# Kernel optimization log

Measured on AMD Instinct MI355X. Metric: run time of the kernel, lower is better.

Reference implementation:

```python
import jax, jax.numpy as jnp
import numpy as np

# yolov5 non_max_suppression defaults (from forward's input_parameters.get defaults)
CONF_THRES = 0.25
IOU_THRES = 0.45
MAX_DET = 1000        # max detections returned per image
TOP_K = 4096          # fixed candidate count entering greedy NMS (jit-friendly stand-in for max_nms)
MAX_WH = 7680.0       # per-class box offset so NMS is class-aware (yolov5 trick)


def setup_inputs() -> dict:
    key = jax.random.key(0)
    k1, k2, k3, k4 = jax.random.split(key, 4)
    B, N, NC = 16, 25200, 80  # 640x640 yolov5 -> 25200 anchors, 80 COCO classes
    xy = jax.random.uniform(k1, (B, N, 2)) * 640.0            # box centers in pixels
    wh = jax.random.uniform(k2, (B, N, 2)) * 160.0 + 4.0       # box sizes
    obj = jax.random.uniform(k3, (B, N, 1))                    # objectness
    cls = jax.random.uniform(k4, (B, N, NC))                   # class scores
    pred = jnp.concatenate([xy, wh, obj, cls], axis=-1)        # [B, N, 85]
    return {"pred": pred}


def _xywh2xyxy(x):
    xy, wh = x[..., :2], x[..., 2:4]
    return jnp.concatenate([xy - wh * 0.5, xy + wh * 0.5], axis=-1)


def _iou_one_vs_all(box, boxes):
    # box [4], boxes [K,4], xyxy
    lt = jnp.maximum(box[:2], boxes[:, :2])
    rb = jnp.minimum(box[2:], boxes[:, 2:])
    wh = jnp.clip(rb - lt, 0.0)
    inter = wh[:, 0] * wh[:, 1]
    a1 = (box[2] - box[0]) * (box[3] - box[1])
    a2 = (boxes[:, 2] - boxes[:, 0]) * (boxes[:, 3] - boxes[:, 1])
    return inter / (a1 + a2 - inter + 1e-7)


def _nms_single(pred):
    # pred [N, 5+nc] raw yolov5 output for one image
    obj = pred[:, 4:5]
    scores_all = pred[:, 5:] * obj                 # conf = obj_conf * cls_conf
    conf = scores_all.max(axis=-1)                 # best-class confidence [N]
    cls = scores_all.argmax(axis=-1).astype(pred.dtype)
    boxes = _xywh2xyxy(pred[:, :4])                # [N,4] xyxy

    valid = conf > CONF_THRES
    s = jnp.where(valid, conf, -1.0)
    order = jnp.argsort(-s)[:TOP_K]                # top candidates by score
    b = boxes[order]                               # [K,4]
    sc = s[order]                                  # [K]
    c = cls[order]                                 # [K]
    ob = b + c[:, None] * MAX_WH                   # class-offset boxes for class-aware NMS

    ar = jnp.arange(TOP_K)

    def step(supp, i):
        alive = (~supp[i]) & (sc[i] > 0.0)
        iou = _iou_one_vs_all(ob[i], ob)
        supp = supp | (alive & (iou > IOU_THRES) & (ar > i))
        return supp, alive

    _, keep = jax.lax.scan(step, jnp.zeros(TOP_K, dtype=bool), ar)

    fs = jnp.where(keep, sc, -1.0)
    idx = jnp.argsort(-fs)[:MAX_DET]               # kept boxes, score-sorted
    det = jnp.concatenate([b[idx], fs[idx][:, None], c[idx][:, None]], axis=-1)  # [max_det,6]
    ok = fs[idx] > 0.0
    return jnp.where(ok[:, None], det, 0.0)        # zero-padded [max_det, 6] (x1,y1,x2,y2,conf,cls)


def reference(pred):
    # [B, max_det, 6] padded detections per image
    return jax.vmap(_nms_single)(pred)
```

## Files before the change

### kernel.cpp

```cpp
#include <hip/hip_runtime.h>

#define BATCH  16
#define NPRED  25200
#define NCLS   80
#define CDIM   85
#define TOPK   4096
#define NPAD   28672
#define NCHUNK 7
#define MAXDET 1000
#define CONF_T 0.25f
#define IOU_T  0.45f
#define MAXWH  7680.0f

typedef unsigned long long u64;
typedef unsigned int u32;
typedef unsigned short u16;
typedef unsigned char u8;

__device__ __forceinline__ u64 umax64(u64 a, u64 b) { return a > b ? a : b; }
__device__ __forceinline__ u64 umin64(u64 a, u64 b) { return a < b ? a : b; }

__device__ __forceinline__ void cx_u64(u64* a, int i, int p, bool desc) {
    u64 x = a[i], y = a[p];
    if (desc ? (x < y) : (x > y)) { a[i] = y; a[p] = x; }
}


__device__ void hybrid_sort4096_desc(u64 r[4], u64* a) {
    const int tid = threadIdx.x;
    for (int k = 2; k <= 4096; k <<= 1) {
        if (k >= 512) {
            int jmax = (k >> 1) > 2048 ? 2048 : (k >> 1);
#pragma unroll
            for (int e = 0; e < 4; ++e) a[4 * tid + e] = r[e];
            __syncthreads();
            for (int j = jmax; j >= 256; j >>= 1) {
#pragma unroll
                for (int t2 = 0; t2 < 2; ++t2) {
                    int q = (t2 << 10) | tid;
                    int i = ((q & ~(j - 1)) << 1) | (q & (j - 1));
                    cx_u64(a, i, i | j, (i & k) == 0);
                }
                __syncthreads();
            }
#pragma unroll
            for (int e = 0; e < 4; ++e) r[e] = a[4 * tid + e];
            __syncthreads();
        }
        {
            int jstart = (k >> 1) > 128 ? 128 : (k >> 1);
            bool desc = (((4 * tid) & k) == 0);
            for (int j = jstart; j >= 4; j >>= 1) {
                int m = j >> 2;
                bool take_max = (((tid & m) == 0) == desc);
#pragma unroll
                for (int e = 0; e < 4; ++e) {
                    u64 v = __shfl_xor(r[e], m, 64);
                    r[e] = take_max ? umax64(r[e], v) : umin64(r[e], v);
                }
            }
        }
        if (k >= 4) {
            bool desc = (((4 * tid) & k) == 0);
            u64 x0 = r[0], x2 = r[2];
            r[0] = desc ? umax64(x0, x2) : umin64(x0, x2);
            r[2] = desc ? umin64(x0, x2) : umax64(x0, x2);
            u64 x1 = r[1], x3 = r[3];
            r[1] = desc ? umax64(x1, x3) : umin64(x1, x3);
            r[3] = desc ? umin64(x1, x3) : umax64(x1, x3);
        }
        {
            bool d01 = (((4 * tid + 0) & k) == 0);
            bool d23 = (((4 * tid + 2) & k) == 0);
            u64 x0 = r[0], x1 = r[1];
            r[0] = d01 ? umax64(x0, x1) : umin64(x0, x1);
            r[1] = d01 ? umin64(x0, x1) : umax64(x0, x1);
            u64 x2 = r[2], x3 = r[3];
            r[2] = d23 ? umax64(x2, x3) : umin64(x2, x3);
            r[3] = d23 ? umin64(x2, x3) : umax64(x2, x3);
        }
    }
}

__device__ void hybrid_merge4096_desc(u64 r[4], u64* a) {
    const int tid = threadIdx.x;
#pragma unroll
    for (int e = 0; e < 4; ++e) a[4 * tid + e] = r[e];
    __syncthreads();
    for (int j = 2048; j >= 256; j >>= 1) {
#pragma unroll
        for (int t2 = 0; t2 < 2; ++t2) {
            int q = (t2 << 10) | tid;
            int i = ((q & ~(j - 1)) << 1) | (q & (j - 1));
            cx_u64(a, i, i | j, true);
        }
        __syncthreads();
    }
#pragma unroll
    for (int e = 0; e < 4; ++e) r[e] = a[4 * tid + e];
    for (int j = 128; j >= 4; j >>= 1) {
        int m = j >> 2;
        bool take_max = ((tid & m) == 0);
#pragma unroll
        for (int e = 0; e < 4; ++e) {
            u64 v = __shfl_xor(r[e], m, 64);
            r[e] = take_max ? umax64(r[e], v) : umin64(r[e], v);
        }
    }
    {
        u64 x0 = r[0], x2 = r[2];
        r[0] = umax64(x0, x2); r[2] = umin64(x0, x2);
        u64 x1 = r[1], x3 = r[3];
        r[1] = umax64(x1, x3); r[3] = umin64(x1, x3);
    }
    {
        u64 x0 = r[0], x1 = r[1];
        r[0] = umax64(x0, x1); r[1] = umin64(x0, x1);
        u64 x2 = r[2], x3 = r[3];
        r[2] = umax64(x2, x3); r[3] = umin64(x2, x3);
    }
}


__global__ __launch_bounds__(256) void k1_score(const float* __restrict__ pred,
                                                u64* __restrict__ keys) {
    const int lane = threadIdx.x & 63;
    const int l16 = lane & 15;
    const long long gw = (long long)blockIdx.x * 4 + (threadIdx.x >> 6);
    const long long rowIdx = gw * 4 + (lane >> 4);
    const int b = (int)(rowIdx / NPAD);
    const int n = (int)(rowIdx - (long long)b * NPAD);
    u64 key = 0ull;
    if (n < NPRED) {
        const float* row = pred + ((long long)b * NPRED + n) * CDIM;
        float obj = row[4];
        u64 m = 0ull;
#pragma unroll
        for (int k = 0; k < 5; ++k) {
            int c = l16 + 16 * k;
            float v = row[5 + c] * obj;
            u64 mk = ((u64)(__float_as_uint(v) | 0x80000000u) << 32) | (u64)(u32)(NCLS - 1 - c);
            if (mk > m) m = mk;
        }
#pragma unroll
        for (int o = 8; o > 0; o >>= 1) {
            u64 other = __shfl_xor(m, o, 64);
            if (other > m) m = other;
        }
        float best = __uint_as_float((u32)(m >> 32) & 0x7FFFFFFFu);
        int cls = (NCLS - 1) - (int)(m & 0x7Fu);
        float s = (best > CONF_T) ? best : -1.0f;
        u32 u = __float_as_uint(s);
        u32 ord = (u & 0x80000000u) ? ~u : (u | 0x80000000u);
        key = ((u64)ord << 32) | ((u64)(u32)(NPAD - 1 - n) << 7) | (u64)(u32)cls;
    }
    if (l16 == 0) keys[(long long)b * NPAD + n] = key;
}


__global__ __launch_bounds__(1024) void k2a_sortchunk(u64* __restrict__ keys) {
    __shared__ u64 a[4096];
    const int tid = threadIdx.x;
    u64* kb = keys + (long long)blockIdx.x * 4096;
    u64 r[4];
#pragma unroll
    for (int e = 0; e < 4; ++e) r[e] = kb[4 * tid + e];
    hybrid_sort4096_desc(r, a);
#pragma unroll
    for (int e = 0; e < 4; ++e) kb[4 * tid + e] = r[e];
}


__global__ __launch_bounds__(1024) void k2m_merge(u64* __restrict__ keys, int stride) {
    __shared__ u64 a[4096];
    const int tid = threadIdx.x;
    const int b = blockIdx.x;
    const int c0 = blockIdx.y * 2 * stride;
    const u64* A = keys + (long long)b * NPAD + (long long)c0 * 4096;
    const u64* B = keys + (long long)b * NPAD + (long long)(c0 + stride) * 4096;
    u64 r[4];
#pragma unroll
    for (int e = 0; e < 4; ++e) {
        int i = 4 * tid + e;
        r[e] = umax64(A[i], B[4095 - i]);
    }
    hybrid_merge4096_desc(r, a);
    u64* O = keys + (long long)b * NPAD + (long long)c0 * 4096;
#pragma unroll
    for (int e = 0; e < 4; ++e) O[4 * tid + e] = r[e];
}


__global__ __launch_bounds__(256) void k3a_build(const float* __restrict__ pred,
                                                 const u64* __restrict__ keys,
                                                 float4* __restrict__ ob,
                                                 u8* __restrict__ clsb,
                                                 u32* __restrict__ count) {
    const int idx = blockIdx.x * 256 + threadIdx.x;
    const int b = idx >> 12;
    const int r = idx & 4095;
    u64 key = keys[(long long)b * NPAD + r];
    u32 hi = (u32)(key >> 32);
    u8 c = 0xFF;
    if (hi > 0x80000000u) {
        int n = (NPAD - 1) - (int)((key >> 7) & 0x7FFFu);
        int ci = (int)(key & 0x7Fu);
        const float* row = pred + ((long long)b * NPRED + n) * CDIM;
        float x = row[0], y = row[1], w = row[2], h = row[3];
        float off = (float)ci * MAXWH;
        float4 o;
        o.x = (x - w * 0.5f) + off;
        o.y = (y - h * 0.5f) + off;
        o.z = (x + w * 0.5f) + off;
        o.w = (y + h * 0.5f) + off;
        ob[idx] = o;
        c = (u8)ci;
        atomicAdd(&count[b * NCLS + ci], 1u);
    }
    clsb[idx] = c;
}


__global__ __launch_bounds__(64) void k3g_gather(const u8* __restrict__ clsb,
                                                 const u32* __restrict__ count,
                                                 u32* __restrict__ startg,
                                                 u16* __restrict__ segIdx) {
    const int b = blockIdx.x;
    const int c = blockIdx.y;
    const int lane = threadIdx.x;
    u32 s = (lane < c) ? count[b * NCLS + lane] : 0u;
    if (lane + 64 < c) s += count[b * NCLS + 64 + lane];
#pragma unroll
    for (int o = 32; o > 0; o >>= 1) s += __shfl_xor(s, o, 64);
    if (lane == 0) startg[b * NCLS + c] = s;
    const u32 base = (u32)b * 4096u;
    u32 pos = s;
    const u64 lt = (1ull << lane) - 1ull;
    for (int it = 0; it < 64; ++it) {
        u8 cc = clsb[base + it * 64 + lane];
        u64 m = __ballot(cc == (u8)c);
        if (cc == (u8)c) {
            int ofs = __popcll(m & lt);
            segIdx[base + pos + ofs] = (u16)(it * 64 + lane);
        }
        pos += (u32)__popcll(m);
    }
}


__global__ __launch_bounds__(64) void k3n_nms(const float4* __restrict__ ob,
                                              const u16* __restrict__ segIdx,
                                              const u32* __restrict__ count,
                                              const u32* __restrict__ startg,
                                              u8* __restrict__ keep,
                                              u8* gsupp_) {
    const int b = blockIdx.x;
    const int c = blockIdx.y;
    const int lane = threadIdx.x;
    const int n = (int)count[b * NCLS + c];
    if (n == 0) return;
    const u32 base = startg[b * NCLS + c];
    __shared__ float4 sbox[1024];
    __shared__ u16 sidx[1024];
    __shared__ u8 ssupp_[1024];
    volatile u8* ssupp = ssupp_;
    volatile u8* gsupp = gsupp_ + b * 4096 + base;
    const float4* obb = ob + b * 4096;
    const u16* seg = segIdx + b * 4096 + base;

    for (int j = lane; j < n && j < 1024; j += 64) {
        int r = seg[j];
        sidx[j] = (u16)r;
        sbox[j] = obb[r];
        ssupp_[j] = 0;
    }
    __syncthreads();

    {
#pragma clang fp contract(off)
        for (int ii = 0; ii < n; ++ii) {
            bool sup = (ii < 1024) ? (ssupp[ii] != 0) : (gsupp[ii] != 0);
            if (sup) continue;
            int ri = (ii < 1024) ? (int)sidx[ii] : (int)seg[ii];
            if (lane == 0) keep[b * 4096 + ri] = 1;
            float4 bi = (ii < 1024) ? sbox[ii] : obb[seg[ii]];
            float a1 = (bi.z - bi.x) * (bi.w - bi.y);
            for (int jj = ii + 1 + lane; jj < n; jj += 64) {
                float4 bj = (jj < 1024) ? sbox[jj] : obb[seg[jj]];
                float ltx = fmaxf(bi.x, bj.x);
                float lty = fmaxf(bi.y, bj.y);
                float rbx = fminf(bi.z, bj.z);
                float rby = fminf(bi.w, bj.w);
                float ww = fmaxf(rbx - ltx, 0.0f);
                float hh = fmaxf(rby - lty, 0.0f);
                float inter = ww * hh;
                float a2 = (bj.z - bj.x) * (bj.w - bj.y);
                float iou = inter / (((a1 + a2) - inter) + 1e-7f);
                if (iou > IOU_T) {
                    if (jj < 1024) ssupp[jj] = 1; else gsupp[jj] = 1;
                }
            }
            __syncthreads();
        }
    }
}


__global__ __launch_bounds__(256) void k3o_out(const float* __restrict__ pred,
                                               const u64* __restrict__ keys,
                                               const u8* __restrict__ keep,
                                               float* __restrict__ out) {
    const int b = blockIdx.x;
    const int tid = threadIdx.x;
    __shared__ u64 words[64];
    __shared__ int wpre[64];
    float* outb = out + (long long)b * MAXDET * 6;
    for (int i = tid; i < MAXDET * 6; i += 256) outb[i] = 0.0f;
    const u8* kp = keep + b * 4096;
    if (tid < 64) {
        u64 w = 0ull;
        const u64* k8 = (const u64*)(kp + tid * 64);
#pragma unroll
        for (int q = 0; q < 8; ++q) {
            u64 v = k8[q];
#pragma unroll
            for (int bb = 0; bb < 8; ++bb)
                if ((v >> (8 * bb)) & 0xFFull) w |= 1ull << (q * 8 + bb);
        }
        words[tid] = w;
    }
    __syncthreads();
    if (tid == 0) {
        int run = 0;
        for (int t = 0; t < 64; ++t) { wpre[t] = run; run += __popcll(words[t]); }
    }
    __syncthreads();
    const u64* kb = keys + (long long)b * NPAD;
    for (int r = tid; r < 4096; r += 256) {
        int wd = r >> 6;
        if ((words[wd] >> (r & 63)) & 1ull) {
            int pos = wpre[wd] + __popcll(words[wd] & ((1ull << (r & 63)) - 1ull));
            if (pos < MAXDET) {
                u64 key = kb[r];
                u32 hi = (u32)(key >> 32);
                int n = (NPAD - 1) - (int)((key >> 7) & 0x7FFFu);
                const float* row = pred + ((long long)b * NPRED + n) * CDIM;
                float x = row[0], y = row[1], w2 = row[2], h = row[3];
                float* o = outb + pos * 6;
                o[0] = x - w2 * 0.5f;
                o[1] = y - h * 0.5f;
                o[2] = x + w2 * 0.5f;
                o[3] = y + h * 0.5f;
                o[4] = __uint_as_float(hi & 0x7FFFFFFFu);
                o[5] = (float)(key & 0x7Fu);
            }
        }
    }
}


extern "C" void kernel_launch(void* const* d_in, const int* in_sizes, int n_in,
                              void* d_out, int out_size, void* d_ws, size_t ws_size,
                              hipStream_t stream) {
    const float* pred = (const float*)d_in[0];
    float* out = (float*)d_out;

    char* ws = (char*)d_ws;
    u64* keys   = (u64*)ws;
    float4* ob  = (float4*)(ws + 3670016);
    u8* clsb    = (u8*)(ws + 4718592);
    u16* segIdx = (u16*)(ws + 4784128);
    u32* startg = (u32*)(ws + 4915200);
    u32* count  = (u32*)(ws + 4920320);
    u8* keep    = (u8*)(ws + 4925440);
    u8* gsupp   = (u8*)(ws + 4990976);
    (void)hipMemsetAsync(ws + 4920320, 0, 136192, stream);

    hipLaunchKernelGGL(k1_score, dim3(BATCH * NPAD / 16), dim3(256), 0, stream, pred, keys);
    hipLaunchKernelGGL(k2a_sortchunk, dim3(BATCH * NCHUNK), dim3(1024), 0, stream, keys);
    hipLaunchKernelGGL(k2m_merge, dim3(BATCH, 3), dim3(1024), 0, stream, keys, 1);
    hipLaunchKernelGGL(k2m_merge, dim3(BATCH, 2), dim3(1024), 0, stream, keys, 2);
    hipLaunchKernelGGL(k2m_merge, dim3(BATCH, 1), dim3(1024), 0, stream, keys, 4);
    hipLaunchKernelGGL(k3a_build, dim3(BATCH * TOPK / 256), dim3(256), 0, stream,
                       pred, keys, ob, clsb, count);
    hipLaunchKernelGGL(k3g_gather, dim3(BATCH, NCLS), dim3(64), 0, stream,
                       clsb, count, startg, segIdx);
    hipLaunchKernelGGL(k3n_nms, dim3(BATCH, NCLS), dim3(64), 0, stream,
                       ob, segIdx, count, startg, keep, gsupp);
    hipLaunchKernelGGL(k3o_out, dim3(BATCH), dim3(256), 0, stream, pred, keys, keep, out);
}
```

Baseline: 304.6 us.

## Replace full candidate sort with histogram threshold selection plus single 4096 sort

The score kernel now builds a per-image 4096-bucket histogram of valid scores with global atomics. A new per-image kernel scans that histogram to find the bucket holding the 4096th candidate, compacts the keys above that bucket into shared memory, and sorts the boundary bucket separately to fill the remainder. Only the selected 4096 keys are then bitonic-sorted, replacing the multi-chunk sort and merge passes over all 28672 padded keys. The trade-offs are atomic contention on the histogram and a single block per image doing the compaction, plus a boundary bucket capped at 1024 entries.

```diff
diff --git a/kernel.cpp b/kernel.cpp
--- a/kernel.cpp
+++ b/kernel.cpp
@@ -5,12 +5,12 @@
 #define NCLS   80
 #define CDIM   85
 #define TOPK   4096
-#define NPAD   28672
-#define NCHUNK 7
+#define NBUCK  4096
 #define MAXDET 1000
 #define CONF_T 0.25f
 #define IOU_T  0.45f
 #define MAXWH  7680.0f
+#define ORD_BASE 0xBE800000u
 
 typedef unsigned long long u64;
 typedef unsigned int u32;
@@ -82,128 +82,196 @@
     }
 }
 
-__device__ void hybrid_merge4096_desc(u64 r[4], u64* a) {
-    const int tid = threadIdx.x;
-#pragma unroll
-    for (int e = 0; e < 4; ++e) a[4 * tid + e] = r[e];
-    __syncthreads();
-    for (int j = 2048; j >= 256; j >>= 1) {
-#pragma unroll
-        for (int t2 = 0; t2 < 2; ++t2) {
-            int q = (t2 << 10) | tid;
-            int i = ((q & ~(j - 1)) << 1) | (q & (j - 1));
-            cx_u64(a, i, i | j, true);
-        }
-        __syncthreads();
-    }
-#pragma unroll
-    for (int e = 0; e < 4; ++e) r[e] = a[4 * tid + e];
-    for (int j = 128; j >= 4; j >>= 1) {
-        int m = j >> 2;
-        bool take_max = ((tid & m) == 0);
-#pragma unroll
-        for (int e = 0; e < 4; ++e) {
-            u64 v = __shfl_xor(r[e], m, 64);
-            r[e] = take_max ? umax64(r[e], v) : umin64(r[e], v);
-        }
-    }
-    {
-        u64 x0 = r[0], x2 = r[2];
-        r[0] = umax64(x0, x2); r[2] = umin64(x0, x2);
-        u64 x1 = r[1], x3 = r[3];
-        r[1] = umax64(x1, x3); r[3] = umin64(x1, x3);
-    }
-    {
-        u64 x0 = r[0], x1 = r[1];
-        r[0] = umax64(x0, x1); r[1] = umin64(x0, x1);
-        u64 x2 = r[2], x3 = r[3];
-        r[2] = umax64(x2, x3); r[3] = umin64(x2, x3);
+__device__ void wave_sort256_desc(u64 r[4]) {
+    const int lane = threadIdx.x & 63;
+    for (int k = 2; k <= 256; k <<= 1) {
+        int jstart = (k >> 1) > 128 ? 128 : (k >> 1);
+        bool desc = (((4 * lane) & k) == 0);
+        for (int j = jstart; j >= 4; j >>= 1) {
+            int m = j >> 2;
+            bool take_max = (((lane & m) == 0) == desc);
+#pragma unroll
+            for (int e = 0; e < 4; ++e) {
+                u64 v = __shfl_xor(r[e], m, 64);
+                r[e] = take_max ? umax64(r[e], v) : umin64(r[e], v);
+            }
+        }
+        if (k >= 4) {
+            u64 x0 = r[0], x2 = r[2];
+            r[0] = desc ? umax64(x0, x2) : umin64(x0, x2);
+            r[2] = desc ? umin64(x0, x2) : umax64(x0, x2);
+            u64 x1 = r[1], x3 = r[3];
+            r[1] = desc ? umax64(x1, x3) : umin64(x1, x3);
+            r[3] = desc ? umin64(x1, x3) : umax64(x1, x3);
+        }
+        {
+            bool d01 = (((4 * lane + 0) & k) == 0);
+            bool d23 = (((4 * lane + 2) & k) == 0);
+            u64 x0 = r[0], x1 = r[1];
+            r[0] = d01 ? umax64(x0, x1) : umin64(x0, x1);
+            r[1] = d01 ? umin64(x0, x1) : umax64(x0, x1);
+            u64 x2 = r[2], x3 = r[3];
+            r[2] = d23 ? umax64(x2, x3) : umin64(x2, x3);
+            r[3] = d23 ? umin64(x2, x3) : umax64(x2, x3);
+        }
     }
 }
 
 
 __global__ __launch_bounds__(256) void k1_score(const float* __restrict__ pred,
-                                                u64* __restrict__ keys) {
+                                                u64* __restrict__ keys,
+                                                u32* __restrict__ ghist) {
     const int lane = threadIdx.x & 63;
     const int l16 = lane & 15;
     const long long gw = (long long)blockIdx.x * 4 + (threadIdx.x >> 6);
     const long long rowIdx = gw * 4 + (lane >> 4);
-    const int b = (int)(rowIdx / NPAD);
-    const int n = (int)(rowIdx - (long long)b * NPAD);
-    u64 key = 0ull;
-    if (n < NPRED) {
-        const float* row = pred + ((long long)b * NPRED + n) * CDIM;
-        float obj = row[4];
-        u64 m = 0ull;
-#pragma unroll
-        for (int k = 0; k < 5; ++k) {
-            int c = l16 + 16 * k;
-            float v = row[5 + c] * obj;
-            u64 mk = ((u64)(__float_as_uint(v) | 0x80000000u) << 32) | (u64)(u32)(NCLS - 1 - c);
-            if (mk > m) m = mk;
-        }
-#pragma unroll
-        for (int o = 8; o > 0; o >>= 1) {
-            u64 other = __shfl_xor(m, o, 64);
-            if (other > m) m = other;
-        }
+    const int b = (int)(rowIdx / NPRED);
+    const int n = (int)(rowIdx - (long long)b * NPRED);
+    const float* row = pred + rowIdx * CDIM;
+    float obj = row[4];
+    u64 m = 0ull;
+#pragma unroll
+    for (int k = 0; k < 5; ++k) {
+        int c = l16 + 16 * k;
+        float v = row[5 + c] * obj;
+        u64 mk = ((u64)(__float_as_uint(v) | 0x80000000u) << 32) | (u64)(u32)(NCLS - 1 - c);
+        if (mk > m) m = mk;
+    }
+#pragma unroll
+    for (int o = 8; o > 0; o >>= 1) {
+        u64 other = __shfl_xor(m, o, 64);
+        if (other > m) m = other;
+    }
+    if (l16 == 0) {
         float best = __uint_as_float((u32)(m >> 32) & 0x7FFFFFFFu);
         int cls = (NCLS - 1) - (int)(m & 0x7Fu);
         float s = (best > CONF_T) ? best : -1.0f;
         u32 u = __float_as_uint(s);
         u32 ord = (u & 0x80000000u) ? ~u : (u | 0x80000000u);
-        key = ((u64)ord << 32) | ((u64)(u32)(NPAD - 1 - n) << 7) | (u64)(u32)cls;
-    }
-    if (l16 == 0) keys[(long long)b * NPAD + n] = key;
-}
-
-
-__global__ __launch_bounds__(1024) void k2a_sortchunk(u64* __restrict__ keys) {
-    __shared__ u64 a[4096];
+        keys[rowIdx] = ((u64)ord << 32) | ((u64)(u32)(32767 - n) << 7) | (u64)(u32)cls;
+        if (ord > ORD_BASE)
+            atomicAdd(&ghist[b * NBUCK + ((ord - ORD_BASE - 1u) >> 12)], 1u);
+    }
+}
+
+
+__global__ __launch_bounds__(1024) void k2cs(const u64* __restrict__ keys,
+                                             const u32* __restrict__ ghist,
+                                             u64* __restrict__ topSorted) {
+    __shared__ u64 smem[4096];
+    __shared__ u64 side[1024];
+    __shared__ u32 wsum[16];
+    __shared__ int sh_T, sh_C1, sh_R, c1pos, sidepos;
+    const int b = blockIdx.x;
     const int tid = threadIdx.x;
-    u64* kb = keys + (long long)blockIdx.x * 4096;
+    const int lane = tid & 63;
+    const int wid = tid >> 6;
+
+    u32 h[4];
+    u32 tsum = 0;
+#pragma unroll
+    for (int e = 0; e < 4; ++e) {
+        h[e] = ghist[b * NBUCK + (NBUCK - 1 - (4 * tid + e))];
+        tsum += h[e];
+    }
+    u32 inc = tsum;
+    for (int o = 1; o < 64; o <<= 1) {
+        u32 v = __shfl_up(inc, o, 64);
+        if (lane >= o) inc += v;
+    }
+    if (lane == 63) wsum[wid] = inc;
+    __syncthreads();
+    if (tid == 0) {
+        u32 run = 0;
+        for (int i = 0; i < 16; ++i) { u32 t = wsum[i]; wsum[i] = run; run += t; }
+        sh_T = -1; sh_C1 = (int)run; sh_R = 0;
+        c1pos = 0; sidepos = 0;
+    }
+    __syncthreads();
+    {
+        u32 cum = wsum[wid] + (inc - tsum);
+#pragma unroll
+        for (int e = 0; e < 4; ++e) {
+            if (h[e] > 0 && cum < (u32)TOPK && cum + h[e] >= (u32)TOPK) {
+                sh_T = NBUCK - 1 - (4 * tid + e);
+                sh_C1 = (int)cum;
+                sh_R = TOPK - (int)cum;
+            }
+            cum += h[e];
+        }
+    }
+    __syncthreads();
+    const int T = sh_T, C1 = sh_C1, R = sh_R;
+
+    for (int i = tid; i < 4096; i += 1024) smem[i] = 0ull;
+    side[tid] = 0ull;
+    __syncthreads();
+    const u64* kb = keys + (long long)b * NPRED;
+    for (int n = tid; n < NPRED; n += 1024) {
+        u64 key = kb[n];
+        u32 hi = (u32)(key >> 32);
+        if (hi > ORD_BASE) {
+            int bt = (int)((hi - ORD_BASE - 1u) >> 12);
+            if (bt > T) {
+                int slot = atomicAdd(&c1pos, 1);
+                smem[slot] = key;
+            } else if (bt == T) {
+                int s2 = atomicAdd(&sidepos, 1);
+                if (s2 < 1024) side[s2] = key;
+            }
+        }
+    }
+    __syncthreads();
+
+    if (R > 0) {
+        int cntT = sidepos;
+        if (cntT <= 256) {
+            if (wid == 0) {
+                u64 r[4];
+#pragma unroll
+                for (int e = 0; e < 4; ++e) r[e] = side[4 * lane + e];
+                wave_sort256_desc(r);
+#pragma unroll
+                for (int e = 0; e < 4; ++e) side[4 * lane + e] = r[e];
+            }
+        } else {
+            for (int k = 2; k <= 1024; k <<= 1) {
+                for (int j = k >> 1; j >= 1; j >>= 1) {
+                    if (tid < 512) {
+                        int q = tid;
+                        int i = ((q & ~(j - 1)) << 1) | (q & (j - 1));
+                        cx_u64(side, i, i | j, (i & k) == 0);
+                    }
+                    __syncthreads();
+                }
+            }
+        }
+        __syncthreads();
+        if (tid < R) smem[C1 + tid] = side[tid];
+    }
+    __syncthreads();
+
     u64 r[4];
 #pragma unroll
-    for (int e = 0; e < 4; ++e) r[e] = kb[4 * tid + e];
-    hybrid_sort4096_desc(r, a);
-#pragma unroll
-    for (int e = 0; e < 4; ++e) kb[4 * tid + e] = r[e];
-}
-
-
-__global__ __launch_bounds__(1024) void k2m_merge(u64* __restrict__ keys, int stride) {
-    __shared__ u64 a[4096];
-    const int tid = threadIdx.x;
-    const int b = blockIdx.x;
-    const int c0 = blockIdx.y * 2 * stride;
-    const u64* A = keys + (long long)b * NPAD + (long long)c0 * 4096;
-    const u64* B = keys + (long long)b * NPAD + (long long)(c0 + stride) * 4096;
-    u64 r[4];
-#pragma unroll
-    for (int e = 0; e < 4; ++e) {
-        int i = 4 * tid + e;
-        r[e] = umax64(A[i], B[4095 - i]);
-    }
-    hybrid_merge4096_desc(r, a);
-    u64* O = keys + (long long)b * NPAD + (long long)c0 * 4096;
-#pragma unroll
-    for (int e = 0; e < 4; ++e) O[4 * tid + e] = r[e];
+    for (int e = 0; e < 4; ++e) r[e] = smem[4 * tid + e];
+    hybrid_sort4096_desc(r, smem);
+#pragma unroll
+    for (int e = 0; e < 4; ++e) topSorted[(long long)b * TOPK + 4 * tid + e] = r[e];
 }
 
 
 __global__ __launch_bounds__(256) void k3a_build(const float* __restrict__ pred,
-                                                 const u64* __restrict__ keys,
+                                                 const u64* __restrict__ topSorted,
                                                  float4* __restrict__ ob,
                                                  u8* __restrict__ clsb,
                                                  u32* __restrict__ count) {
     const int idx = blockIdx.x * 256 + threadIdx.x;
     const int b = idx >> 12;
-    const int r = idx & 4095;
-    u64 key = keys[(long long)b * NPAD + r];
+    u64 key = topSorted[idx];
     u32 hi = (u32)(key >> 32);
     u8 c = 0xFF;
     if (hi > 0x80000000u) {
-        int n = (NPAD - 1) - (int)((key >> 7) & 0x7FFFu);
+        int n = 32767 - (int)((key >> 7) & 0x7FFFu);
         int ci = (int)(key & 0x7Fu);
         const float* row = pred + ((long long)b * NPRED + n) * CDIM;
         float x = row[0], y = row[1], w = row[2], h = row[3];
@@ -307,7 +375,7 @@
 
 
 __global__ __launch_bounds__(256) void k3o_out(const float* __restrict__ pred,
-                                               const u64* __restrict__ keys,
+                                               const u64* __restrict__ topSorted,
                                                const u8* __restrict__ keep,
                                                float* __restrict__ out) {
     const int b = blockIdx.x;
@@ -335,7 +403,7 @@
         for (int t = 0; t < 64; ++t) { wpre[t] = run; run += __popcll(words[t]); }
     }
     __syncthreads();
-    const u64* kb = keys + (long long)b * NPAD;
+    const u64* kb = topSorted + (long long)b * TOPK;
     for (int r = tid; r < 4096; r += 256) {
         int wd = r >> 6;
         if ((words[wd] >> (r & 63)) & 1ull) {
@@ -343,7 +411,7 @@
             if (pos < MAXDET) {
                 u64 key = kb[r];
                 u32 hi = (u32)(key >> 32);
-                int n = (NPAD - 1) - (int)((key >> 7) & 0x7FFFu);
+                int n = 32767 - (int)((key >> 7) & 0x7FFFu);
                 const float* row = pred + ((long long)b * NPRED + n) * CDIM;
                 float x = row[0], y = row[1], w2 = row[2], h = row[3];
                 float* o = outb + pos * 6;
@@ -366,26 +434,26 @@
     float* out = (float*)d_out;
 
     char* ws = (char*)d_ws;
-    u64* keys   = (u64*)ws;
-    float4* ob  = (float4*)(ws + 3670016);
-    u8* clsb    = (u8*)(ws + 4718592);
-    u16* segIdx = (u16*)(ws + 4784128);
-    u32* startg = (u32*)(ws + 4915200);
-    u32* count  = (u32*)(ws + 4920320);
-    u8* keep    = (u8*)(ws + 4925440);
-    u8* gsupp   = (u8*)(ws + 4990976);
-    (void)hipMemsetAsync(ws + 4920320, 0, 136192, stream);
-
-    hipLaunchKernelGGL(k1_score, dim3(BATCH * NPAD / 16), dim3(256), 0, stream, pred, keys);
-    hipLaunchKernelGGL(k2a_sortchunk, dim3(BATCH * NCHUNK), dim3(1024), 0, stream, keys);
-    hipLaunchKernelGGL(k2m_merge, dim3(BATCH, 3), dim3(1024), 0, stream, keys, 1);
-    hipLaunchKernelGGL(k2m_merge, dim3(BATCH, 2), dim3(1024), 0, stream, keys, 2);
-    hipLaunchKernelGGL(k2m_merge, dim3(BATCH, 1), dim3(1024), 0, stream, keys, 4);
+    u64* keys      = (u64*)ws;
+    u64* topSorted = (u64*)(ws + 3225600);
+    float4* ob     = (float4*)(ws + 3749888);
+    u8* clsb       = (u8*)(ws + 4798464);
+    u16* segIdx    = (u16*)(ws + 4864000);
+    u32* startg    = (u32*)(ws + 4995072);
+    u32* ghist     = (u32*)(ws + 5000192);
+    u32* count     = (u32*)(ws + 5262336);
+    u8* keep       = (u8*)(ws + 5267456);
+    u8* gsupp      = (u8*)(ws + 5332992);
+    (void)hipMemsetAsync(ws + 5000192, 0, 398336, stream);
+
+    hipLaunchKernelGGL(k1_score, dim3(BATCH * NPRED / 16), dim3(256), 0, stream,
+                       pred, keys, ghist);
+    hipLaunchKernelGGL(k2cs, dim3(BATCH), dim3(1024), 0, stream, keys, ghist, topSorted);
     hipLaunchKernelGGL(k3a_build, dim3(BATCH * TOPK / 256), dim3(256), 0, stream,
-                       pred, keys, ob, clsb, count);
+                       pred, topSorted, ob, clsb, count);
     hipLaunchKernelGGL(k3g_gather, dim3(BATCH, NCLS), dim3(64), 0, stream,
                        clsb, count, startg, segIdx);
     hipLaunchKernelGGL(k3n_nms, dim3(BATCH, NCLS), dim3(64), 0, stream,
                        ob, segIdx, count, startg, keep, gsupp);
-    hipLaunchKernelGGL(k3o_out, dim3(BATCH), dim3(256), 0, stream, pred, keys, keep, out);
-}
+    hipLaunchKernelGGL(k3o_out, dim3(BATCH), dim3(256), 0, stream, pred, topSorted, keep, out);
+}
```

New measurement: 301.1 us. Within noise of the previous version (-1.2%).
